# Optimization experiments

Measured on AMD Instinct MI355X. Metric: run time of the kernel, lower is better.

Reference implementation:

```python
import jax, jax.numpy as jnp
import numpy as np

DIM = 768      # embedding dim
NH = 12        # num heads
HD = DIM // NH # head dim = 64
WS = 7         # window size
BASE = 100.0   # rope base
TAU = 0.01     # cosine attention temperature


def _rope_tables(Wn):
    # 2D RoPE: first half of head_dim rotates with row index, second half with col index.
    quarter = HD // 4
    inv = BASE ** (-2.0 * jnp.arange(quarter, dtype=jnp.float32) / (HD // 2))  # [HD/4]
    yy, xx = jnp.meshgrid(jnp.arange(Wn, dtype=jnp.float32),
                          jnp.arange(Wn, dtype=jnp.float32), indexing='ij')
    ang = jnp.concatenate([yy.reshape(-1, 1) * inv, xx.reshape(-1, 1) * inv], axis=-1)  # [W^2, HD/2]
    return jnp.sin(ang), jnp.cos(ang)


def _apply_rope(t, sin, cos):
    # t: [Bw, L, nH, HD]; rotate-half within each spatial-axis block
    h = HD // 2
    t1, t2 = t[..., :h], t[..., h:]
    s = sin[None, :, None, :]
    c = cos[None, :, None, :]
    return jnp.concatenate([t1 * c - t2 * s, t1 * s + t2 * c], axis=-1)


def setup_inputs() -> dict:
    key = jax.random.key(0)
    k1, k2, k3 = jax.random.split(key, 3)
    B, H, W_img = 2, 224, 224
    x = jax.random.normal(k1, (B, H * W_img, DIM), jnp.float32)
    qkv_w = jax.random.normal(k2, (3 * DIM, DIM), jnp.float32) * 0.02
    proj_w = jax.random.normal(k3, (DIM, DIM), jnp.float32) * 0.02
    return {"x": x, "qkv_w": qkv_w, "proj_w": proj_w, "H": H, "W_img": W_img, "shift": 1}


def reference(x, qkv_w, proj_w, H, W_img, shift):
    B, N, D = x.shape
    Wn = WS
    x2d = x.reshape(B, H, W_img, D)
    ss = Wn // 2 if shift else 0
    if shift:
        x2d = jnp.roll(x2d, (-ss, -ss), axis=(1, 2))
    pad_b = (-H) % Wn
    pad_r = (-W_img) % Wn
    if pad_b or pad_r:
        x2d = jnp.pad(x2d, ((0, 0), (0, pad_b), (0, pad_r), (0, 0)))
    Hp, Wp = H + pad_b, W_img + pad_r
    # window partition: [B, Hp, Wp, D] -> [B*nW, W^2, D]
    xw = x2d.reshape(B, Hp // Wn, Wn, Wp // Wn, Wn, D).transpose(0, 1, 3, 2, 4, 5).reshape(-1, Wn * Wn, D)
    Bw, L = xw.shape[0], Wn * Wn
    qkv = xw @ qkv_w.T                       # [Bw, L, 3D]
    q, k, v = jnp.split(qkv, 3, axis=-1)
    q = q.reshape(Bw, L, NH, HD)
    k = k.reshape(Bw, L, NH, HD)
    v = v.reshape(Bw, L, NH, HD)
    sin, cos = _rope_tables(Wn)
    q = _apply_rope(q, sin, cos)
    k = _apply_rope(k, sin, cos)
    # cosine attention: L2-normalize q,k then scale by 1/tau
    q = q / jnp.clip(jnp.linalg.norm(q, axis=-1, keepdims=True), 1e-12)
    k = k / jnp.clip(jnp.linalg.norm(k, axis=-1, keepdims=True), 1e-12)
    q = q.transpose(0, 2, 1, 3)  # [Bw, nH, L, HD]
    k = k.transpose(0, 2, 1, 3)
    v = v.transpose(0, 2, 1, 3)
    attn = jax.nn.softmax(jnp.einsum('bhqd,bhkd->bhqk', q, k) / TAU, axis=-1)
    out = jnp.einsum('bhqk,bhkd->bhqd', attn, v)
    out = out.transpose(0, 2, 1, 3).reshape(Bw, L, D)
    # window reverse
    out = out.reshape(B, Hp // Wn, Wp // Wn, Wn, Wn, D).transpose(0, 1, 3, 2, 4, 5).reshape(B, Hp, Wp, D)
    out = out[:, :H, :W_img, :]
    if shift:
        out = jnp.roll(out, (ss, ss), axis=(1, 2))
    return out.reshape(B, N, D) @ proj_w.T
```

## Files before the change

kernel.cpp:

```cpp
#include <hip/hip_runtime.h>
#include <cstdint>
#include <cstddef>

typedef __bf16 bf16x8 __attribute__((ext_vector_type(8)));
typedef float  f32x4  __attribute__((ext_vector_type(4)));

typedef __attribute__((address_space(1))) void v_as1;
typedef __attribute__((address_space(3))) void v_as3;

#define NTOK 100352
#define DIMC 768
#define NHEAD 12
#define IMG 224
#define WN 7
#define WL 49

__device__ __forceinline__ unsigned short f2bf(float f) {
    uint32_t u = __float_as_uint(f);
    uint32_t r = (u + 0x7FFFu + ((u >> 16) & 1u)) >> 16;
    return (unsigned short)r;
}
__device__ __forceinline__ float bf2f(unsigned short u) {
    return __uint_as_float(((uint32_t)u) << 16);
}

__device__ __forceinline__ void async_cp16(const void* g, void* l) {
    __builtin_amdgcn_global_load_lds((v_as1*)g, (v_as3*)l, 16, 0, 0);
}

__global__ __launch_bounds__(256) void hilo_kernel(const float* __restrict__ in,
        unsigned short* __restrict__ hi, unsigned short* __restrict__ lo,
        int n4, int has_lo) {
    int idx = blockIdx.x * 256 + threadIdx.x;
    int stride = gridDim.x * 256;
    for (int i = idx; i < n4; i += stride) {
        float4 v = reinterpret_cast<const float4*>(in)[i];
        ushort4 h;
        h.x = f2bf(v.x); h.y = f2bf(v.y); h.z = f2bf(v.z); h.w = f2bf(v.w);
        reinterpret_cast<ushort4*>(hi)[i] = h;
        if (has_lo) {
            ushort4 l;
            l.x = f2bf(v.x - bf2f(h.x));
            l.y = f2bf(v.y - bf2f(h.y));
            l.z = f2bf(v.z - bf2f(h.z));
            l.w = f2bf(v.w - bf2f(h.w));
            reinterpret_cast<ushort4*>(lo)[i] = l;
        }
    }
}

#define BM 128
#define BN 128
#define BK 32
template <int TRIPLE>
__global__ __launch_bounds__(256) void gemm_bt(
    const unsigned short* __restrict__ Ahi, const unsigned short* __restrict__ Alo,
    const unsigned short* __restrict__ Bhi, const unsigned short* __restrict__ Blo,
    float* __restrict__ Cf, unsigned short* __restrict__ Cb,
    int M, int N, int K)
{
    __shared__ unsigned short lAh[BM * BK];
    __shared__ unsigned short lBh[BN * BK];
    __shared__ unsigned short lAl[BM * BK];
    __shared__ unsigned short lBl[BN * BK];

    const int tid  = threadIdx.x;
    const int wave = tid >> 6;
    const int lane = tid & 63;

    const int nTiles = N / BN;
    const int bm = blockIdx.x / nTiles;
    const int bn = blockIdx.x % nTiles;
    const int m0 = bm * BM, n0 = bn * BN;

    const int wm = (wave & 1) * 64;
    const int wn = (wave >> 1) * 64;

    f32x4 acc[4][4];
#pragma unroll
    for (int i = 0; i < 4; i++)
#pragma unroll
        for (int j = 0; j < 4; j++) acc[i][j] = (f32x4){0.f, 0.f, 0.f, 0.f};

    const int c0 = tid, c1 = tid + 256;
    const int ar0 = c0 >> 2, ac0 = (c0 & 3) * 8;
    const int ar1 = c1 >> 2, ac1 = (c1 & 3) * 8;
    const size_t off0 = (size_t)(wave * 64) * 8;
    const size_t off1 = (size_t)(256 + wave * 64) * 8;

    const int lquad = lane >> 4;
    const int l16   = lane & 15;

    const unsigned short* AhB = Ahi + (size_t)m0 * K;
    const unsigned short* BhB = Bhi + (size_t)n0 * K;
    const unsigned short* AlB = TRIPLE ? Alo + (size_t)m0 * K : nullptr;
    const unsigned short* BlB = TRIPLE ? Blo + (size_t)n0 * K : nullptr;

    for (int kk = 0; kk < K; kk += BK) {
        async_cp16(AhB + (size_t)ar0 * K + kk + ac0, &lAh[off0]);
        async_cp16(AhB + (size_t)ar1 * K + kk + ac1, &lAh[off1]);
        async_cp16(BhB + (size_t)ar0 * K + kk + ac0, &lBh[off0]);
        async_cp16(BhB + (size_t)ar1 * K + kk + ac1, &lBh[off1]);
        if (TRIPLE) {
            async_cp16(AlB + (size_t)ar0 * K + kk + ac0, &lAl[off0]);
            async_cp16(AlB + (size_t)ar1 * K + kk + ac1, &lAl[off1]);
            async_cp16(BlB + (size_t)ar0 * K + kk + ac0, &lBl[off0]);
            async_cp16(BlB + (size_t)ar1 * K + kk + ac1, &lBl[off1]);
        }
        __syncthreads();
        bf16x8 ah[4], bh[4];
#pragma unroll
        for (int i = 0; i < 4; i++)
            ah[i] = *reinterpret_cast<const bf16x8*>(&lAh[(size_t)(wm + i * 16 + l16) * BK + lquad * 8]);
#pragma unroll
        for (int j = 0; j < 4; j++)
            bh[j] = *reinterpret_cast<const bf16x8*>(&lBh[(size_t)(wn + j * 16 + l16) * BK + lquad * 8]);
#pragma unroll
        for (int i = 0; i < 4; i++)
#pragma unroll
            for (int j = 0; j < 4; j++)
                acc[i][j] = __builtin_amdgcn_mfma_f32_16x16x32_bf16(ah[i], bh[j], acc[i][j], 0, 0, 0);
        if (TRIPLE) {
            bf16x8 al[4], bl[4];
#pragma unroll
            for (int i = 0; i < 4; i++)
                al[i] = *reinterpret_cast<const bf16x8*>(&lAl[(size_t)(wm + i * 16 + l16) * BK + lquad * 8]);
#pragma unroll
            for (int j = 0; j < 4; j++)
                bl[j] = *reinterpret_cast<const bf16x8*>(&lBl[(size_t)(wn + j * 16 + l16) * BK + lquad * 8]);
#pragma unroll
            for (int i = 0; i < 4; i++)
#pragma unroll
                for (int j = 0; j < 4; j++) {
                    acc[i][j] = __builtin_amdgcn_mfma_f32_16x16x32_bf16(al[i], bh[j], acc[i][j], 0, 0, 0);
                    acc[i][j] = __builtin_amdgcn_mfma_f32_16x16x32_bf16(ah[i], bl[j], acc[i][j], 0, 0, 0);
                }
        }
        __syncthreads();
    }

    if (Cf) {
#pragma unroll
        for (int i = 0; i < 4; i++) {
            int rb = m0 + wm + i * 16 + lquad * 4;
#pragma unroll
            for (int r = 0; r < 4; r++) {
                float* crow = Cf + (size_t)(rb + r) * N + n0 + wn + l16;
#pragma unroll
                for (int j = 0; j < 4; j++) crow[j * 16] = acc[i][j][r];
            }
        }
    } else {
#pragma unroll
        for (int i = 0; i < 4; i++) {
            int rb = m0 + wm + i * 16 + lquad * 4;
#pragma unroll
            for (int r = 0; r < 4; r++) {
                unsigned short* crow = Cb + (size_t)(rb + r) * N + n0 + wn + l16;
#pragma unroll
                for (int j = 0; j < 4; j++) crow[j * 16] = f2bf(acc[i][j][r]);
            }
        }
    }
}

#define QBM 256
#define QBN 256
#define QBK 32

__global__ __launch_bounds__(512) void gemm_qk(
    const unsigned short* __restrict__ Ahi, const unsigned short* __restrict__ Alo,
    const unsigned short* __restrict__ Bhi, const unsigned short* __restrict__ Blo,
    float* __restrict__ C, int M, int N, int K)
{
    __shared__ __align__(16) unsigned short lA[2][2][QBM * QBK];
    __shared__ __align__(16) unsigned short lB[2][2][QBN * QBK];

    const int tid  = threadIdx.x;
    const int wave = tid >> 6;
    const int lane = tid & 63;
    const int l16  = lane & 15;
    const int lq   = lane >> 4;

    const int nwg = gridDim.x;
    const int cpx = nwg >> 3;
    const int bid = blockIdx.x;
    const int wg  = (bid & 7) * cpx + (bid >> 3);

    const int nTiles = N / QBN;
    const int bm = wg / nTiles, bn = wg % nTiles;
    const int m0 = bm * QBM, n0 = bn * QBN;

    const int wm = (wave >> 2) * 128;
    const int wn = (wave & 3) * 64;

    const unsigned short* Ah = Ahi + (size_t)m0 * K;
    const unsigned short* Al = Alo + (size_t)m0 * K;
    const unsigned short* Bh = Bhi + (size_t)n0 * K;
    const unsigned short* Bl = Blo + (size_t)n0 * K;

    const size_t goff0 = (size_t)(tid >> 2) * K + (size_t)(tid & 3) * 8;
    const size_t goff1 = goff0 + (size_t)128 * K;
    const int s0e = wave * 512;
    const int s1e = 4096 + wave * 512;

    const int NT = K / QBK;

    f32x4 acc[8][4];
#pragma unroll
    for (int i = 0; i < 8; i++)
#pragma unroll
        for (int j = 0; j < 4; j++) acc[i][j] = (f32x4){0.f, 0.f, 0.f, 0.f};

#define STG(dst, gb, kk) do { \
        async_cp16((gb) + goff0 + (size_t)(kk), &(dst)[s0e]); \
        async_cp16((gb) + goff1 + (size_t)(kk), &(dst)[s1e]); } while (0)

#define PBAR do { asm volatile("" ::: "memory"); \
        __builtin_amdgcn_s_barrier(); \
        asm volatile("" ::: "memory"); } while (0)

#define LGW0 do { asm volatile("s_waitcnt lgkmcnt(0)" ::: "memory"); \
        __builtin_amdgcn_sched_barrier(0); } while (0)

#define MF(H, G) do { \
    _Pragma("unroll") for (int ii = 0; ii < 4; ++ii) { \
      _Pragma("unroll") for (int jj = 0; jj < 2; ++jj) { \
        const int j = (G) * 2 + jj; \
        f32x4 a = acc[(H) * 4 + ii][j]; \
        a = __builtin_amdgcn_mfma_f32_16x16x32_bf16(ah[ii], bh[j], a, 0, 0, 0); \
        a = __builtin_amdgcn_mfma_f32_16x16x32_bf16(al[ii], bh[j], a, 0, 0, 0); \
        a = __builtin_amdgcn_mfma_f32_16x16x32_bf16(ah[ii], bl[j], a, 0, 0, 0); \
        acc[(H) * 4 + ii][j] = a; } } } while (0)

    STG(lA[0][0], Ah, 0); STG(lA[0][1], Al, 0);
    STG(lB[0][0], Bh, 0); STG(lB[0][1], Bl, 0);
    STG(lB[1][1], Bl, QBK);
    asm volatile("s_waitcnt vmcnt(2)" ::: "memory");
    PBAR;

#define TILE(T, CUR, NXT) do { \
    bf16x8 ah[4], al[4], bh[4], bl[4]; \
     \
    _Pragma("unroll") for (int j = 0; j < 4; ++j) { \
        bh[j] = *reinterpret_cast<const bf16x8*>(&lB[CUR][0][(wn + j * 16 + l16) * QBK + lq * 8]); \
        bl[j] = *reinterpret_cast<const bf16x8*>(&lB[CUR][1][(wn + j * 16 + l16) * QBK + lq * 8]); } \
    _Pragma("unroll") for (int ii = 0; ii < 4; ++ii) { \
        ah[ii] = *reinterpret_cast<const bf16x8*>(&lA[CUR][0][(wm + ii * 16 + l16) * QBK + lq * 8]); \
        al[ii] = *reinterpret_cast<const bf16x8*>(&lA[CUR][1][(wm + ii * 16 + l16) * QBK + lq * 8]); } \
    if ((T) + 1 < NT) STG(lA[NXT][0], Ah, ((T) + 1) * QBK); \
    PBAR; LGW0; \
    __builtin_amdgcn_s_setprio(1); MF(0, 0); __builtin_amdgcn_s_setprio(0); \
    PBAR; \
     \
    if ((T) + 1 < NT) STG(lA[NXT][1], Al, ((T) + 1) * QBK); \
    PBAR; \
    __builtin_amdgcn_s_setprio(1); MF(0, 1); __builtin_amdgcn_s_setprio(0); \
    PBAR; \
     \
    _Pragma("unroll") for (int ii = 0; ii < 4; ++ii) { \
        ah[ii] = *reinterpret_cast<const bf16x8*>(&lA[CUR][0][(wm + 64 + ii * 16 + l16) * QBK + lq * 8]); \
        al[ii] = *reinterpret_cast<const bf16x8*>(&lA[CUR][1][(wm + 64 + ii * 16 + l16) * QBK + lq * 8]); } \
    if ((T) + 1 < NT) STG(lB[NXT][0], Bh, ((T) + 1) * QBK); \
    PBAR; LGW0; \
    __builtin_amdgcn_s_setprio(1); MF(1, 1); __builtin_amdgcn_s_setprio(0); \
    PBAR; \
     \
    if ((T) + 2 < NT) STG(lB[CUR][1], Bl, ((T) + 2) * QBK); \
    PBAR; \
    __builtin_amdgcn_s_setprio(1); MF(1, 0); __builtin_amdgcn_s_setprio(0); \
    if ((T) + 1 < NT) { \
        if ((T) + 2 < NT) { asm volatile("s_waitcnt vmcnt(2)" ::: "memory"); } \
        else              { asm volatile("s_waitcnt vmcnt(0)" ::: "memory"); } \
    } \
    PBAR; \
} while (0)

    for (int t = 0; t < NT; t += 2) {
        TILE(t, 0, 1);
        TILE(t + 1, 1, 0);
    }

#undef TILE
#undef MF
#undef LGW0
#undef PBAR
#undef STG

#pragma unroll
    for (int i = 0; i < 8; ++i) {
        const int rb = m0 + wm + i * 16 + lq * 4;
#pragma unroll
        for (int r = 0; r < 4; ++r) {
            float* crow = C + (size_t)(rb + r) * N + n0 + wn + l16;
#pragma unroll
            for (int j = 0; j < 4; ++j) crow[j * 16] = acc[i][j][r];
        }
    }
}

__global__ __launch_bounds__(256) void attn_kernel(
    const float* __restrict__ qk,
    const unsigned short* __restrict__ vbuf,
    unsigned short* __restrict__ attnout)
{
    const int h   = blockIdx.x % NHEAD;
    const int win = blockIdx.x / NHEAD;
    const int b   = win >> 10;
    const int wy  = (win >> 5) & 31;
    const int wx  = win & 31;

    __shared__ __align__(16) float sq[52][68];
    __shared__ __align__(16) float sk[52][68];
    __shared__ __align__(16) unsigned short sv[52][68];
    __shared__ __align__(16) float sS[52][52];
    __shared__ float rsum[WL];
    __shared__ int   rowidx[WL];

    const int tid = threadIdx.x;

    if (tid < WL) {
        int i = tid / WN, j = tid % WN;
        int ys = (wy * WN + i + 3) % IMG;
        int xs = (wx * WN + j + 3) % IMG;
        rowidx[tid] = b * (IMG * IMG) + ys * IMG + xs;
    }
    __syncthreads();

    const float LOG2_100_D16 = 0.41524101186092f;
    {
        const int hw = tid >> 5;
        const int t  = tid & 31;
        for (int pass = 0; pass < 7; ++pass) {
            int l = pass * 8 + hw;
            if (l < 49) {
                int i = l / WN, j = l % WN;
                float pos = (t < 16) ? (float)i : (float)j;
                float ang = pos * exp2f(-(float)(t & 15) * LOG2_100_D16);
                float s, c;
                __sincosf(ang, &s, &c);
                size_t base = (size_t)rowidx[l] * 1536 + h * 64;
                float q1 = qk[base + t], q2 = qk[base + t + 32];
                float k1 = qk[base + 768 + t], k2 = qk[base + 768 + t + 32];
                float nq = q1 * q1 + q2 * q2;
                float nk = k1 * k1 + k2 * k2;
#pragma unroll
                for (int m = 1; m < 32; m <<= 1) {
                    nq += __shfl_xor(nq, m);
                    nk += __shfl_xor(nk, m);
                }
                float iq = 10.f / fmaxf(sqrtf(nq), 1e-12f);
                float ik = 10.f / fmaxf(sqrtf(nk), 1e-12f);
                sq[l][t]      = (q1 * c - q2 * s) * iq;
                sq[l][t + 32] = (q1 * s + q2 * c) * iq;
                sk[l][t]      = (k1 * c - k2 * s) * ik;
                sk[l][t + 32] = (k1 * s + k2 * c) * ik;
            } else if (l < 52) {
                sq[l][t] = 0.f; sq[l][t + 32] = 0.f;
                sk[l][t] = 0.f; sk[l][t + 32] = 0.f;
            }
        }
    }
    for (int e = tid; e < 52 * 64; e += 256) {
        int l = e >> 6, d = e & 63;
        sv[l][d] = (l < 49) ? vbuf[(size_t)rowidx[l] * 768 + h * 64 + d] : (unsigned short)0;
    }
    __syncthreads();

    if (tid < 169) {
        int ta = tid / 13, tb = tid - ta * 13;
        int a0 = ta * 4, b0 = tb * 4;
        float acc[4][4];
#pragma unroll
        for (int i = 0; i < 4; i++)
#pragma unroll
            for (int j = 0; j < 4; j++) acc[i][j] = 0.f;
#pragma unroll 4
        for (int d4 = 0; d4 < 16; ++d4) {
            float4 qa[4], kb[4];
#pragma unroll
            for (int i = 0; i < 4; i++) qa[i] = *reinterpret_cast<const float4*>(&sq[a0 + i][d4 * 4]);
#pragma unroll
            for (int j = 0; j < 4; j++) kb[j] = *reinterpret_cast<const float4*>(&sk[b0 + j][d4 * 4]);
#pragma unroll
            for (int i = 0; i < 4; i++)
#pragma unroll
                for (int j = 0; j < 4; j++)
                    acc[i][j] += qa[i].x * kb[j].x + qa[i].y * kb[j].y +
                                 qa[i].z * kb[j].z + qa[i].w * kb[j].w;
        }
#pragma unroll
        for (int i = 0; i < 4; i++) {
            float4 r;
            r.x = (b0 + 0 < WL) ? acc[i][0] : -1e30f;
            r.y = (b0 + 1 < WL) ? acc[i][1] : -1e30f;
            r.z = (b0 + 2 < WL) ? acc[i][2] : -1e30f;
            r.w = (b0 + 3 < WL) ? acc[i][3] : -1e30f;
            *reinterpret_cast<float4*>(&sS[a0 + i][b0]) = r;
        }
    }
    __syncthreads();

    if (tid < WL * 4) {
        int a = tid >> 2, s4 = tid & 3;
        float m = -1e30f;
        for (int bb = s4; bb < WL; bb += 4) m = fmaxf(m, sS[a][bb]);
        m = fmaxf(m, __shfl_xor(m, 1));
        m = fmaxf(m, __shfl_xor(m, 2));
        float sum = 0.f;
        for (int bb = s4; bb < WL; bb += 4) {
            float p = __expf(sS[a][bb] - m);
            sS[a][bb] = p;
            sum += p;
        }
        sum += __shfl_xor(sum, 1);
        sum += __shfl_xor(sum, 2);
        if (s4 == 0) rsum[a] = 1.f / sum;
    }
    __syncthreads();

    if (tid < 208) {
        int ta = tid >> 4, td = tid & 15;
        int a0 = ta * 4, d0 = td * 4;
        float acc[4][4];
#pragma unroll
        for (int i = 0; i < 4; i++)
#pragma unroll
            for (int j = 0; j < 4; j++) acc[i][j] = 0.f;
        for (int bb = 0; bb < WL; ++bb) {
            float p0 = sS[a0 + 0][bb], p1 = sS[a0 + 1][bb];
            float p2 = sS[a0 + 2][bb], p3 = sS[a0 + 3][bb];
            ushort4 vr = *reinterpret_cast<const ushort4*>(&sv[bb][d0]);
            float v0 = bf2f(vr.x), v1 = bf2f(vr.y), v2 = bf2f(vr.z), v3 = bf2f(vr.w);
            acc[0][0] += p0 * v0; acc[0][1] += p0 * v1; acc[0][2] += p0 * v2; acc[0][3] += p0 * v3;
            acc[1][0] += p1 * v0; acc[1][1] += p1 * v1; acc[1][2] += p1 * v2; acc[1][3] += p1 * v3;
            acc[2][0] += p2 * v0; acc[2][1] += p2 * v1; acc[2][2] += p2 * v2; acc[2][3] += p2 * v3;
            acc[3][0] += p3 * v0; acc[3][1] += p3 * v1; acc[3][2] += p3 * v2; acc[3][3] += p3 * v3;
        }
#pragma unroll
        for (int i = 0; i < 4; i++) {
            int a = a0 + i;
            if (a < WL) {
                float r = rsum[a];
                ushort4 o;
                o.x = f2bf(acc[i][0] * r);
                o.y = f2bf(acc[i][1] * r);
                o.z = f2bf(acc[i][2] * r);
                o.w = f2bf(acc[i][3] * r);
                *reinterpret_cast<ushort4*>(&attnout[(size_t)rowidx[a] * 768 + h * 64 + d0]) = o;
            }
        }
    }
}

extern "C" void kernel_launch(void* const* d_in, const int* in_sizes, int n_in,
                              void* d_out, int out_size, void* d_ws, size_t ws_size,
                              hipStream_t stream) {
    const float* x      = (const float*)d_in[0];
    const float* qkv_w  = (const float*)d_in[1];
    const float* proj_w = (const float*)d_in[2];
    float* out = (float*)d_out;

    char* ws = (char*)d_ws;
    const size_t XE    = (size_t)NTOK * DIMC;
    const size_t WQKV  = (size_t)3 * DIMC * DIMC;
    const size_t WPROJ = (size_t)DIMC * DIMC;

    unsigned short* x_hi = (unsigned short*)ws;
    unsigned short* x_lo = x_hi + XE;
    unsigned short* w_hi = x_lo + XE;
    unsigned short* w_lo = w_hi + WQKV;
    unsigned short* p_hi = w_lo + WQKV;
    float* qkbuf = (float*)(p_hi + WPROJ);
    unsigned short* vbuf    = x_lo;
    unsigned short* attnout = x_hi;

    size_t need = (size_t)((char*)(qkbuf + (size_t)NTOK * 1536) - ws);
    if (ws_size < need) return;

    hilo_kernel<<<8192, 256, 0, stream>>>(x, x_hi, x_lo, (int)(XE / 4), 1);
    hilo_kernel<<<1728, 256, 0, stream>>>(qkv_w, w_hi, w_lo, (int)(WQKV / 4), 1);
    hilo_kernel<<<576, 256, 0, stream>>>(proj_w, p_hi, (unsigned short*)nullptr, (int)(WPROJ / 4), 0);

    gemm_qk<<<(NTOK / 256) * (1536 / 256), 512, 0, stream>>>(
        x_hi, x_lo, w_hi, w_lo, qkbuf, NTOK, 1536, DIMC);
    gemm_bt<0><<<(NTOK / 128) * (768 / 128), 256, 0, stream>>>(
        x_hi, (unsigned short*)nullptr, w_hi + (size_t)1536 * DIMC, (unsigned short*)nullptr,
        (float*)nullptr, vbuf, NTOK, 768, DIMC);

    attn_kernel<<<2048 * NHEAD, 256, 0, stream>>>(qkbuf, vbuf, attnout);

    gemm_bt<0><<<(NTOK / 128) * (768 / 128), 256, 0, stream>>>(
        attnout, (unsigned short*)nullptr, p_hi, (unsigned short*)nullptr,
        out, (unsigned short*)nullptr, NTOK, 768, DIMC);
}
```

Measured before the change: 2.322 ms.

## Move window attention QK and PV products onto split-bf16 MFMA with swizzled LDS

Replaces the scalar FP32 QK^T and PV loops in the attention kernel with 16x16x32 bf16 MFMA instructions. Operands are split into hi/lo bf16 pairs to keep near-fp32 accuracy, and tiles are padded to 64 with XOR-swizzled shared-memory layouts. V is now loaded from global memory early into registers, then transposed into LDS, and the Q/K buffers are reused for P and V^T. This is meant to cut the ALU cost of the per-window attention. The trade-offs are extra MFMA passes for precision, more conversion work, and narrower scalar bf16 output stores.

Result: faster. 2.000 ms (-13.9%).

```diff
diff --git a/kernel.cpp b/kernel.cpp
--- a/kernel.cpp
+++ b/kernel.cpp
@@ -4,6 +4,7 @@
 
 typedef __bf16 bf16x8 __attribute__((ext_vector_type(8)));
 typedef float  f32x4  __attribute__((ext_vector_type(4)));
+typedef unsigned short us8 __attribute__((ext_vector_type(8)));
 
 typedef __attribute__((address_space(1))) void v_as1;
 typedef __attribute__((address_space(3))) void v_as3;
@@ -241,7 +242,6 @@
 
 #define TILE(T, CUR, NXT) do { \
     bf16x8 ah[4], al[4], bh[4], bl[4]; \
-     \
     _Pragma("unroll") for (int j = 0; j < 4; ++j) { \
         bh[j] = *reinterpret_cast<const bf16x8*>(&lB[CUR][0][(wn + j * 16 + l16) * QBK + lq * 8]); \
         bl[j] = *reinterpret_cast<const bf16x8*>(&lB[CUR][1][(wn + j * 16 + l16) * QBK + lq * 8]); } \
@@ -252,12 +252,10 @@
     PBAR; LGW0; \
     __builtin_amdgcn_s_setprio(1); MF(0, 0); __builtin_amdgcn_s_setprio(0); \
     PBAR; \
-     \
     if ((T) + 1 < NT) STG(lA[NXT][1], Al, ((T) + 1) * QBK); \
     PBAR; \
     __builtin_amdgcn_s_setprio(1); MF(0, 1); __builtin_amdgcn_s_setprio(0); \
     PBAR; \
-     \
     _Pragma("unroll") for (int ii = 0; ii < 4; ++ii) { \
         ah[ii] = *reinterpret_cast<const bf16x8*>(&lA[CUR][0][(wm + 64 + ii * 16 + l16) * QBK + lq * 8]); \
         al[ii] = *reinterpret_cast<const bf16x8*>(&lA[CUR][1][(wm + 64 + ii * 16 + l16) * QBK + lq * 8]); } \
@@ -265,7 +263,6 @@
     PBAR; LGW0; \
     __builtin_amdgcn_s_setprio(1); MF(1, 1); __builtin_amdgcn_s_setprio(0); \
     PBAR; \
-     \
     if ((T) + 2 < NT) STG(lB[CUR][1], Bl, ((T) + 2) * QBK); \
     PBAR; \
     __builtin_amdgcn_s_setprio(1); MF(1, 0); __builtin_amdgcn_s_setprio(0); \
@@ -310,14 +307,24 @@
     const int wy  = (win >> 5) & 31;
     const int wx  = win & 31;
 
-    __shared__ __align__(16) float sq[52][68];
-    __shared__ __align__(16) float sk[52][68];
-    __shared__ __align__(16) unsigned short sv[52][68];
-    __shared__ __align__(16) float sS[52][52];
+    __shared__ __align__(16) unsigned short qh[64 * 64];
+    __shared__ __align__(16) unsigned short ql[64 * 64];
+    __shared__ __align__(16) unsigned short kh[64 * 64];
+    __shared__ __align__(16) unsigned short kl[64 * 64];
+    __shared__ __align__(16) float sS[64 * 64];
     __shared__ float rsum[WL];
     __shared__ int   rowidx[WL];
 
-    const int tid = threadIdx.x;
+    unsigned short* Ph = qh;
+    unsigned short* Pl = ql;
+    unsigned short* Vt = kh;
+
+    const int tid  = threadIdx.x;
+    const int wave = tid >> 6;
+    const int lane = tid & 63;
+    const int l16  = lane & 15;
+    const int lq   = lane >> 4;
+    const int wm16 = wave * 16;
 
     if (tid < WL) {
         int i = tid / WN, j = tid % WN;
@@ -327,13 +334,20 @@
     }
     __syncthreads();
 
+    const int vl = tid >> 2, vd0 = (tid & 3) * 16;
+    us8 vr0 = (us8)0, vr1 = (us8)0;
+    if (tid < 196) {
+        const us8* vp = reinterpret_cast<const us8*>(vbuf + (size_t)rowidx[vl] * 768 + h * 64 + vd0);
+        vr0 = vp[0]; vr1 = vp[1];
+    }
+
     const float LOG2_100_D16 = 0.41524101186092f;
     {
         const int hw = tid >> 5;
         const int t  = tid & 31;
-        for (int pass = 0; pass < 7; ++pass) {
+        for (int pass = 0; pass < 8; ++pass) {
             int l = pass * 8 + hw;
-            if (l < 49) {
+            if (l < WL) {
                 int i = l / WN, j = l % WN;
                 float pos = (t < 16) ? (float)i : (float)j;
                 float ang = pos * exp2f(-(float)(t & 15) * LOG2_100_D16);
@@ -351,66 +365,81 @@
                 }
                 float iq = 10.f / fmaxf(sqrtf(nq), 1e-12f);
                 float ik = 10.f / fmaxf(sqrtf(nk), 1e-12f);
-                sq[l][t]      = (q1 * c - q2 * s) * iq;
-                sq[l][t + 32] = (q1 * s + q2 * c) * iq;
-                sk[l][t]      = (k1 * c - k2 * s) * ik;
-                sk[l][t + 32] = (k1 * s + k2 * c) * ik;
-            } else if (l < 52) {
-                sq[l][t] = 0.f; sq[l][t + 32] = 0.f;
-                sk[l][t] = 0.f; sk[l][t + 32] = 0.f;
-            }
-        }
-    }
-    for (int e = tid; e < 52 * 64; e += 256) {
-        int l = e >> 6, d = e & 63;
-        sv[l][d] = (l < 49) ? vbuf[(size_t)rowidx[l] * 768 + h * 64 + d] : (unsigned short)0;
+                float qv1 = (q1 * c - q2 * s) * iq;
+                float qv2 = (q1 * s + q2 * c) * iq;
+                float kv1 = (k1 * c - k2 * s) * ik;
+                float kv2 = (k1 * s + k2 * c) * ik;
+                const int rb = l << 6, sw = (l & 7) << 3;
+                int e1 = rb + (t ^ sw);
+                int e2 = rb + ((t + 32) ^ sw);
+                unsigned short hv;
+                hv = f2bf(qv1); qh[e1] = hv; ql[e1] = f2bf(qv1 - bf2f(hv));
+                hv = f2bf(qv2); qh[e2] = hv; ql[e2] = f2bf(qv2 - bf2f(hv));
+                hv = f2bf(kv1); kh[e1] = hv; kl[e1] = f2bf(kv1 - bf2f(hv));
+                hv = f2bf(kv2); kh[e2] = hv; kl[e2] = f2bf(kv2 - bf2f(hv));
+            } else if (l < 64) {
+                const int rb = l << 6, sw = (l & 7) << 3;
+                int e1 = rb + (t ^ sw);
+                int e2 = rb + ((t + 32) ^ sw);
+                qh[e1] = 0; ql[e1] = 0; qh[e2] = 0; ql[e2] = 0;
+                kh[e1] = 0; kl[e1] = 0; kh[e2] = 0; kl[e2] = 0;
+            }
+        }
     }
     __syncthreads();
 
-    if (tid < 169) {
-        int ta = tid / 13, tb = tid - ta * 13;
-        int a0 = ta * 4, b0 = tb * 4;
-        float acc[4][4];
-#pragma unroll
-        for (int i = 0; i < 4; i++)
-#pragma unroll
-            for (int j = 0; j < 4; j++) acc[i][j] = 0.f;
-#pragma unroll 4
-        for (int d4 = 0; d4 < 16; ++d4) {
-            float4 qa[4], kb[4];
-#pragma unroll
-            for (int i = 0; i < 4; i++) qa[i] = *reinterpret_cast<const float4*>(&sq[a0 + i][d4 * 4]);
-#pragma unroll
-            for (int j = 0; j < 4; j++) kb[j] = *reinterpret_cast<const float4*>(&sk[b0 + j][d4 * 4]);
-#pragma unroll
-            for (int i = 0; i < 4; i++)
-#pragma unroll
-                for (int j = 0; j < 4; j++)
-                    acc[i][j] += qa[i].x * kb[j].x + qa[i].y * kb[j].y +
-                                 qa[i].z * kb[j].z + qa[i].w * kb[j].w;
-        }
-#pragma unroll
-        for (int i = 0; i < 4; i++) {
-            float4 r;
-            r.x = (b0 + 0 < WL) ? acc[i][0] : -1e30f;
-            r.y = (b0 + 1 < WL) ? acc[i][1] : -1e30f;
-            r.z = (b0 + 2 < WL) ? acc[i][2] : -1e30f;
-            r.w = (b0 + 3 < WL) ? acc[i][3] : -1e30f;
-            *reinterpret_cast<float4*>(&sS[a0 + i][b0]) = r;
+    {
+        f32x4 accq[4];
+#pragma unroll
+        for (int j = 0; j < 4; j++) accq[j] = (f32x4){0.f, 0.f, 0.f, 0.f};
+
+        bf16x8 ah[2], al[2];
+        const int arow = wm16 + l16;
+        const int asw = (arow & 7) << 3;
+#pragma unroll
+        for (int s = 0; s < 2; ++s) {
+            int e = (arow << 6) + ((s * 32 + lq * 8) ^ asw);
+            ah[s] = *reinterpret_cast<const bf16x8*>(&qh[e]);
+            al[s] = *reinterpret_cast<const bf16x8*>(&ql[e]);
+        }
+#pragma unroll
+        for (int j = 0; j < 4; ++j) {
+            const int brow = j * 16 + l16;
+            const int bsw = (brow & 7) << 3;
+#pragma unroll
+            for (int s = 0; s < 2; ++s) {
+                int e = (brow << 6) + ((s * 32 + lq * 8) ^ bsw);
+                bf16x8 bh = *reinterpret_cast<const bf16x8*>(&kh[e]);
+                bf16x8 bl = *reinterpret_cast<const bf16x8*>(&kl[e]);
+                accq[j] = __builtin_amdgcn_mfma_f32_16x16x32_bf16(ah[s], bh, accq[j], 0, 0, 0);
+                accq[j] = __builtin_amdgcn_mfma_f32_16x16x32_bf16(al[s], bh, accq[j], 0, 0, 0);
+                accq[j] = __builtin_amdgcn_mfma_f32_16x16x32_bf16(ah[s], bl, accq[j], 0, 0, 0);
+            }
+        }
+#pragma unroll
+        for (int j = 0; j < 4; ++j) {
+#pragma unroll
+            for (int r = 0; r < 4; ++r) {
+                int row = wm16 + lq * 4 + r;
+                int e = (row << 6) + ((j * 16 + l16) ^ ((row & 7) << 2));
+                sS[e] = accq[j][r];
+            }
         }
     }
     __syncthreads();
 
     if (tid < WL * 4) {
         int a = tid >> 2, s4 = tid & 3;
+        const int rb = a << 6, sw = (a & 7) << 2;
         float m = -1e30f;
-        for (int bb = s4; bb < WL; bb += 4) m = fmaxf(m, sS[a][bb]);
+        for (int bb = s4; bb < WL; bb += 4) m = fmaxf(m, sS[rb + (bb ^ sw)]);
         m = fmaxf(m, __shfl_xor(m, 1));
         m = fmaxf(m, __shfl_xor(m, 2));
         float sum = 0.f;
         for (int bb = s4; bb < WL; bb += 4) {
-            float p = __expf(sS[a][bb] - m);
-            sS[a][bb] = p;
+            int e = rb + (bb ^ sw);
+            float p = __expf(sS[e] - m);
+            sS[e] = p;
             sum += p;
         }
         sum += __shfl_xor(sum, 1);
@@ -419,35 +448,72 @@
     }
     __syncthreads();
 
-    if (tid < 208) {
-        int ta = tid >> 4, td = tid & 15;
-        int a0 = ta * 4, d0 = td * 4;
-        float acc[4][4];
-#pragma unroll
-        for (int i = 0; i < 4; i++)
-#pragma unroll
-            for (int j = 0; j < 4; j++) acc[i][j] = 0.f;
-        for (int bb = 0; bb < WL; ++bb) {
-            float p0 = sS[a0 + 0][bb], p1 = sS[a0 + 1][bb];
-            float p2 = sS[a0 + 2][bb], p3 = sS[a0 + 3][bb];
-            ushort4 vr = *reinterpret_cast<const ushort4*>(&sv[bb][d0]);
-            float v0 = bf2f(vr.x), v1 = bf2f(vr.y), v2 = bf2f(vr.z), v3 = bf2f(vr.w);
-            acc[0][0] += p0 * v0; acc[0][1] += p0 * v1; acc[0][2] += p0 * v2; acc[0][3] += p0 * v3;
-            acc[1][0] += p1 * v0; acc[1][1] += p1 * v1; acc[1][2] += p1 * v2; acc[1][3] += p1 * v3;
-            acc[2][0] += p2 * v0; acc[2][1] += p2 * v1; acc[2][2] += p2 * v2; acc[2][3] += p2 * v3;
-            acc[3][0] += p3 * v0; acc[3][1] += p3 * v1; acc[3][2] += p3 * v2; acc[3][3] += p3 * v3;
-        }
-#pragma unroll
-        for (int i = 0; i < 4; i++) {
-            int a = a0 + i;
-            if (a < WL) {
-                float r = rsum[a];
-                ushort4 o;
-                o.x = f2bf(acc[i][0] * r);
-                o.y = f2bf(acc[i][1] * r);
-                o.z = f2bf(acc[i][2] * r);
-                o.w = f2bf(acc[i][3] * r);
-                *reinterpret_cast<ushort4*>(&attnout[(size_t)rowidx[a] * 768 + h * 64 + d0]) = o;
+    {
+        const int q = tid >> 2, l0 = (tid & 3) << 4;
+        const int sw32 = (q & 7) << 2, sw16 = (q & 7) << 3;
+#pragma unroll
+        for (int g = 0; g < 4; ++g) {
+            int l = l0 + g * 4;
+            float4 pv = *reinterpret_cast<const float4*>(&sS[(q << 6) + (l ^ sw32)]);
+            ushort4 hb, lb;
+            hb.x = f2bf(pv.x); lb.x = f2bf(pv.x - bf2f(hb.x));
+            hb.y = f2bf(pv.y); lb.y = f2bf(pv.y - bf2f(hb.y));
+            hb.z = f2bf(pv.z); lb.z = f2bf(pv.z - bf2f(hb.z));
+            hb.w = f2bf(pv.w); lb.w = f2bf(pv.w - bf2f(hb.w));
+            int e = (q << 6) + (l ^ sw16);
+            *reinterpret_cast<ushort4*>(&Ph[e]) = hb;
+            *reinterpret_cast<ushort4*>(&Pl[e]) = lb;
+        }
+    }
+    if (tid < 196) {
+#pragma unroll
+        for (int i = 0; i < 8; ++i) {
+            int d = vd0 + i;
+            Vt[(d << 6) + (vl ^ ((d & 7) << 3))] = vr0[i];
+        }
+#pragma unroll
+        for (int i = 0; i < 8; ++i) {
+            int d = vd0 + 8 + i;
+            Vt[(d << 6) + (vl ^ ((d & 7) << 3))] = vr1[i];
+        }
+    }
+    __syncthreads();
+
+    {
+        f32x4 acco[4];
+#pragma unroll
+        for (int j = 0; j < 4; j++) acco[j] = (f32x4){0.f, 0.f, 0.f, 0.f};
+
+        bf16x8 ph[2], pl[2];
+        const int arow = wm16 + l16;
+        const int asw = (arow & 7) << 3;
+#pragma unroll
+        for (int s = 0; s < 2; ++s) {
+            int e = (arow << 6) + ((s * 32 + lq * 8) ^ asw);
+            ph[s] = *reinterpret_cast<const bf16x8*>(&Ph[e]);
+            pl[s] = *reinterpret_cast<const bf16x8*>(&Pl[e]);
+        }
+#pragma unroll
+        for (int j = 0; j < 4; ++j) {
+            const int drow = j * 16 + l16;
+            const int dsw = (drow & 7) << 3;
+#pragma unroll
+            for (int s = 0; s < 2; ++s) {
+                int e = (drow << 6) + ((s * 32 + lq * 8) ^ dsw);
+                bf16x8 vv = *reinterpret_cast<const bf16x8*>(&Vt[e]);
+                acco[j] = __builtin_amdgcn_mfma_f32_16x16x32_bf16(ph[s], vv, acco[j], 0, 0, 0);
+                acco[j] = __builtin_amdgcn_mfma_f32_16x16x32_bf16(pl[s], vv, acco[j], 0, 0, 0);
+            }
+        }
+#pragma unroll
+        for (int r = 0; r < 4; ++r) {
+            int q = wm16 + lq * 4 + r;
+            if (q < WL) {
+                float rv = rsum[q];
+                size_t gbase = (size_t)rowidx[q] * 768 + h * 64;
+#pragma unroll
+                for (int j = 0; j < 4; ++j)
+                    attnout[gbase + j * 16 + l16] = f2bf(acco[j][r] * rv);
             }
         }
     }
```
